# Kernel tuning notes

Hardware: AMD Instinct MI355X
Metric: run time of the kernel (lower is better)

Reference implementation:

```python
import jax, jax.numpy as jnp
import numpy as np

EPS = 1e-6
GROUPS = 8


def setup_inputs() -> dict:
    key = jax.random.key(0)
    ks = jax.random.split(key, 8)
    B, C, H, W = 4, 128, 64, 64
    s = 1.0 / np.sqrt(C)
    return {
        "x": jax.random.normal(ks[0], (B, C, H, W), jnp.float32),
        "gn_scale": jnp.ones((C,), jnp.float32),
        "gn_bias": jnp.zeros((C,), jnp.float32),
        "wq": jax.random.normal(ks[1], (C, C), jnp.float32) * s,
        "bq": jnp.zeros((C,), jnp.float32),
        "wk": jax.random.normal(ks[2], (C, C), jnp.float32) * s,
        "bk": jnp.zeros((C,), jnp.float32),
        "wv": jax.random.normal(ks[3], (C, C), jnp.float32) * s,
        "bv": jnp.zeros((C,), jnp.float32),
        "wp": jax.random.normal(ks[4], (C, C), jnp.float32) * s,
        "bp": jnp.zeros((C,), jnp.float32),
    }


def _group_norm(x, scale, bias):
    B, C, H, W = x.shape
    g = x.reshape(B, GROUPS, C // GROUPS, H * W)
    mu = g.mean(axis=(2, 3), keepdims=True)
    var = g.var(axis=(2, 3), keepdims=True)
    g = (g - mu) * jax.lax.rsqrt(var + EPS)
    g = g.reshape(B, C, H, W)
    return g * scale[None, :, None, None] + bias[None, :, None, None]


def reference(x, gn_scale, gn_bias, wq, bq, wk, bk, wv, bv, wp, bp):
    B, C, H, W = x.shape
    N = H * W
    h = _group_norm(x, gn_scale, gn_bias).reshape(B, C, N)
    # 1x1 convs == channel matmuls: (C_out, C_in) x (B, C_in, N)
    q = jnp.einsum('oc,bcn->bon', wq, h) + bq[None, :, None]
    k = jnp.einsum('oc,bcn->bon', wk, h) + bk[None, :, None]
    v = jnp.einsum('oc,bcn->bon', wv, h) + bv[None, :, None]
    # scores: (B, N, N), w[b,n,m] = sum_c q[b,c,n] k[b,c,m]
    w = jnp.einsum('bcn,bcm->bnm', q, k) * (C ** -0.5)
    w = jax.nn.softmax(w, axis=-1)
    # h_[b,c,n] = sum_m w[b,n,m] v[b,c,m]
    h_ = jnp.einsum('bnm,bcm->bcn', w, v)
    out = jnp.einsum('oc,bcn->bon', wp, h_) + bp[None, :, None]
    return x + out.reshape(B, C, H, W)
```

## Files before the change

kernel.cpp:

```cpp
#include <hip/hip_runtime.h>
#include <math.h>

#define B_ 4
#define C_ 128
#define N_ 4096
#define NSPLIT 4
#define MT 32
#define PLD 40
#define HLD 136
#define VTLD 24

typedef float floatx4 __attribute__((ext_vector_type(4)));
typedef short bf16x8 __attribute__((ext_vector_type(8)));

__device__ __forceinline__ ushort f2bf(float f) {
  unsigned u = __float_as_uint(f);
  return (ushort)((u + 0x7FFF + ((u >> 16) & 1)) >> 16);
}
__device__ __forceinline__ float bf2f(ushort u) {
  return __uint_as_float(((unsigned)u) << 16);
}
__device__ __forceinline__ unsigned pkbf(float a, float b) {
  return __builtin_amdgcn_perm(__float_as_uint(a) + 0x8000u,
                               __float_as_uint(b) + 0x8000u, 0x07060302u);
}
__device__ __forceinline__ float fexp2(float x) {
#if __has_builtin(__builtin_amdgcn_exp2f)
  return __builtin_amdgcn_exp2f(x);
#else
  return exp2f(x);
#endif
}
__device__ __forceinline__ void gl2lds16(const ushort* g, ushort* l) {
  __builtin_amdgcn_global_load_lds(
      (const __attribute__((address_space(1))) void*)g,
      (__attribute__((address_space(3))) void*)l, 16, 0, 0);
}

__global__ __launch_bounds__(256) void prep_kernel(
    const float* __restrict__ x, float* __restrict__ gstat,
    const float* __restrict__ wq, const float* __restrict__ wk,
    const float* __restrict__ wv, const float* __restrict__ wp,
    ushort* __restrict__ wB) {
  if (blockIdx.x >= 256) {
    int i = (blockIdx.x - 256) * 256 + threadIdx.x;
    int m = i >> 14, j = i & 16383;
    const float* src = (m == 0) ? wq : (m == 1) ? wk : (m == 2) ? wv : wp;
    wB[i] = f2bf(src[j]);
    return;
  }
  int b = blockIdx.x >> 6, g = (blockIdx.x >> 3) & 7, part = blockIdx.x & 7;
  const float4* xp = (const float4*)(x + (size_t)(b * C_ + g * 16) * N_) + part * 2048;
  float s = 0.f, ss = 0.f;
  for (int i = threadIdx.x; i < 2048; i += 256) {
    float4 v = xp[i];
    s += v.x + v.y + v.z + v.w;
    ss += v.x * v.x + v.y * v.y + v.z * v.z + v.w * v.w;
  }
  #pragma unroll
  for (int o = 32; o > 0; o >>= 1) {
    s += __shfl_down(s, o, 64);
    ss += __shfl_down(ss, o, 64);
  }
  __shared__ float rs[4], rss[4];
  int wid = threadIdx.x >> 6, lane = threadIdx.x & 63;
  if (lane == 0) { rs[wid] = s; rss[wid] = ss; }
  __syncthreads();
  if (threadIdx.x == 0) {
    int slot = (b * 8 + g) * 8 + part;
    gstat[slot]       = rs[0] + rs[1] + rs[2] + rs[3];
    gstat[256 + slot] = rss[0] + rss[1] + rss[2] + rss[3];
  }
}

__global__ __launch_bounds__(256) void gnqkv_kernel(
    const float* __restrict__ x, const float* __restrict__ gstat,
    const float* __restrict__ scale, const float* __restrict__ bias,
    const ushort* __restrict__ wB,
    const float* __restrict__ bq, const float* __restrict__ bk,
    const float* __restrict__ bv,
    ushort* __restrict__ qT, ushort* __restrict__ kT, ushort* __restrict__ vB) {
  __shared__ __align__(16) ushort hs[16][HLD];
  __shared__ __align__(16) ushort Qt[16][HLD];
  __shared__ __align__(16) ushort Kt[16][HLD];
  __shared__ __align__(16) ushort Vt[128][VTLD];
  __shared__ float sSc[C_], sBi[C_];
  int tid = threadIdx.x;
  int b = blockIdx.x >> 8;
  int n0 = (blockIdx.x & 255) * 16;
  if (tid < 128) {
    int g = tid >> 4;
    float S = 0.f, SS = 0.f;
    #pragma unroll
    for (int p = 0; p < 8; ++p) {
      S  += gstat[(b * 8 + g) * 8 + p];
      SS += gstat[256 + (b * 8 + g) * 8 + p];
    }
    float mu = S * (1.f / 65536.f);
    float var = SS * (1.f / 65536.f) - mu * mu;
    float rstd = rsqrtf(var + 1e-6f);
    float sc = scale[tid] * rstd;
    sSc[tid] = sc;
    sBi[tid] = bias[tid] - mu * sc;
  }
  __syncthreads();
  #pragma unroll
  for (int k2 = 0; k2 < 2; ++k2) {
    int i = tid + k2 * 256;
    int c = i >> 2, n4 = i & 3;
    float4 v = *(const float4*)(x + (size_t)(b * C_ + c) * N_ + n0 + n4 * 4);
    float sc = sSc[c], bi = sBi[c];
    hs[n4 * 4 + 0][c] = f2bf(v.x * sc + bi);
    hs[n4 * 4 + 1][c] = f2bf(v.y * sc + bi);
    hs[n4 * 4 + 2][c] = f2bf(v.z * sc + bi);
    hs[n4 * 4 + 3][c] = f2bf(v.w * sc + bi);
  }
  __syncthreads();
  int lane = tid & 63, w = tid >> 6;
  int col = lane & 15, quad = lane >> 4;
  int oh = w * 32;
  bf16x8 hf[4];
  #pragma unroll
  for (int kc = 0; kc < 4; ++kc)
    hf[kc] = *(const bf16x8*)&hs[col][kc * 32 + quad * 8];
  const ushort* Wq = wB;
  const ushort* Wk = wB + 16384;
  const ushort* Wv = wB + 32768;
  const float scl = 0.12751879752224991f;
  #pragma unroll
  for (int ot = 0; ot < 2; ++ot) {
    int o0 = oh + ot * 16;
    floatx4 aq = (floatx4)0.f, ak = (floatx4)0.f, av = (floatx4)0.f;
    #pragma unroll
    for (int kc = 0; kc < 4; ++kc) {
      int wo = (o0 + col) * C_ + kc * 32 + quad * 8;
      aq = __builtin_amdgcn_mfma_f32_16x16x32_bf16(*(const bf16x8*)&Wq[wo], hf[kc], aq, 0, 0, 0);
      ak = __builtin_amdgcn_mfma_f32_16x16x32_bf16(*(const bf16x8*)&Wk[wo], hf[kc], ak, 0, 0, 0);
      av = __builtin_amdgcn_mfma_f32_16x16x32_bf16(*(const bf16x8*)&Wv[wo], hf[kc], av, 0, 0, 0);
    }
    float4 bqv = *(const float4*)&bq[o0 + quad * 4];
    float4 bkv = *(const float4*)&bk[o0 + quad * 4];
    float4 bvv = *(const float4*)&bv[o0 + quad * 4];
    uint2 qs = { pkbf((aq[1] + bqv.y) * scl, (aq[0] + bqv.x) * scl),
                 pkbf((aq[3] + bqv.w) * scl, (aq[2] + bqv.z) * scl) };
    uint2 ks = { pkbf(ak[1] + bkv.y, ak[0] + bkv.x),
                 pkbf(ak[3] + bkv.w, ak[2] + bkv.z) };
    *(uint2*)&Qt[col][o0 + quad * 4] = qs;
    *(uint2*)&Kt[col][o0 + quad * 4] = ks;
    float vv[4] = {av[0] + bvv.x, av[1] + bvv.y, av[2] + bvv.z, av[3] + bvv.w};
    #pragma unroll
    for (int r = 0; r < 4; ++r)
      Vt[o0 + quad * 4 + r][col] = f2bf(vv[r]);
  }
  __syncthreads();
  {
    int row = tid >> 4, seg = tid & 15;
    size_t dst = ((size_t)b * N_ + n0 + row) * C_ + seg * 8;
    *(uint4*)(qT + dst) = *(const uint4*)&Qt[row][seg * 8];
    *(uint4*)(kT + dst) = *(const uint4*)&Kt[row][seg * 8];
  }
  {
    int o = tid >> 1, seg = tid & 1;
    *(uint4*)(vB + ((size_t)b * C_ + o) * N_ + n0 + seg * 8) = *(const uint4*)&Vt[o][seg * 8];
  }
}

__global__ __launch_bounds__(512, 4) void attn_kernel(
    const ushort* __restrict__ qT, const ushort* __restrict__ kT,
    const ushort* __restrict__ vB, ushort* __restrict__ Op,
    float* __restrict__ Lv) {
  __shared__ __align__(16) ushort Ks[2][MT * 128];
  __shared__ __align__(16) ushort Vs[2][C_ * MT];
  __shared__ __align__(16) ushort Ps[2][128 * PLD];
  __shared__ float lpart[8][2][16];
  int sp = blockIdx.x & 3;
  int qblk = (blockIdx.x >> 2) & 31;
  int b = blockIdx.x >> 7;
  int n0 = qblk * 128;
  int tid = threadIdx.x, lane = tid & 63, w = tid >> 6;
  int col = lane & 15, quad = lane >> 4;
  int wu = __builtin_amdgcn_readfirstlane(w);
  int mtw = w & 1, qg = w >> 1;
  int qh = w & 1, cq = w >> 1;
  const ushort* kTb = kT + (size_t)b * N_ * C_;
  const ushort* vBb = vB + (size_t)b * C_ * N_;

  bf16x8 qf[2][4];
  #pragma unroll
  for (int qt = 0; qt < 2; ++qt)
    #pragma unroll
    for (int kc = 0; kc < 4; ++kc)
      qf[qt][kc] = *(const bf16x8*)(qT + ((size_t)b * N_ + n0 + qg * 32 + qt * 16 + col) * C_ + kc * 32 + quad * 8);

  floatx4 Oacc[4][2];
  #pragma unroll
  for (int qt = 0; qt < 4; ++qt)
    #pragma unroll
    for (int ct = 0; ct < 2; ++ct) Oacc[qt][ct] = (floatx4)0.f;
  float lacc[2] = {0.f, 0.f};

  const int m00 = sp * 1024;

  const ushort* kgp;
  const ushort* vgp;
  {
    int r = wu * 4 + (lane >> 4);
    int pos = (lane & 15) ^ (r & 7);
    kgp = kTb + (size_t)(m00 + r) * 128 + pos * 8;
    int c = wu * 16 + (lane >> 2);
    int mc = (lane & 3) ^ ((lane >> 3) & 3);
    vgp = vBb + (size_t)c * N_ + m00 + mc * 8;
  }

  #define STAGE(buf)                                   \
    {                                                  \
      gl2lds16(kgp, &Ks[buf][wu * 512]);               \
      gl2lds16(vgp, &Vs[buf][wu * 512]);               \
      kgp += MT * 128;                                 \
      vgp += MT;                                       \
    }

  #define S_COMPUTE(KsB, st)                                                          \
    {                                                                                 \
      int row = mtw * 16 + col;                                                       \
      bf16x8 kf[4];                                                                   \
      _Pragma("unroll")                                                               \
      for (int kc = 0; kc < 4; ++kc)                                                  \
        kf[kc] = *(const bf16x8*)&(KsB)[row * 128 + (((4 * kc + quad) ^ (col & 7)) * 8)]; \
      __builtin_amdgcn_s_setprio(1);                                                  \
      _Pragma("unroll")                                                               \
      for (int qt = 0; qt < 2; ++qt) {                                                \
        floatx4 acc = (floatx4)0.f;                                                   \
        _Pragma("unroll")                                                             \
        for (int kc = 0; kc < 4; ++kc)                                                \
          acc = __builtin_amdgcn_mfma_f32_16x16x32_bf16(kf[kc], qf[qt][kc], acc, 0, 0, 0); \
        st[qt] = acc;                                                                 \
      }                                                                               \
      __builtin_amdgcn_s_setprio(0);                                                  \
    }

  #define SOFTMAX_WRITE(PsB, st)                                                      \
    {                                                                                 \
      _Pragma("unroll")                                                               \
      for (int qt = 0; qt < 2; ++qt) {                                                \
        int prow = (qg * 32 + qt * 16 + col) * PLD + mtw * 16;                        \
        float p0 = fexp2(st[qt][0]);                                                  \
        float p1 = fexp2(st[qt][1]);                                                  \
        float p2 = fexp2(st[qt][2]);                                                  \
        float p3 = fexp2(st[qt][3]);                                                  \
        uint2 pk = { pkbf(p1, p0), pkbf(p3, p2) };                                    \
        *(uint2*)&(PsB)[prow + quad * 4] = pk;                                        \
        lacc[qt] += (p0 + p1) + (p2 + p3);                                            \
      }                                                                               \
    }

  #define V_LOAD(VsB, vfp)                                                            \
    {                                                                                 \
      _Pragma("unroll")                                                               \
      for (int ct = 0; ct < 2; ++ct)                                                  \
        vfp[ct] = *(const bf16x8*)&(VsB)[(cq * 32 + ct * 16 + col) * MT +             \
                                         ((quad ^ ((col >> 1) & 3)) * 8)];            \
    }

  #define PV_COMPUTE(PsB, vfp)                                                        \
    {                                                                                 \
      __builtin_amdgcn_s_setprio(1);                                                  \
      _Pragma("unroll")                                                               \
      for (int qt = 0; qt < 4; ++qt) {                                                \
        bf16x8 pf = *(const bf16x8*)&(PsB)[(qh * 64 + qt * 16 + col) * PLD + quad * 8]; \
        _Pragma("unroll")                                                             \
        for (int ct = 0; ct < 2; ++ct)                                                \
          Oacc[qt][ct] = __builtin_amdgcn_mfma_f32_16x16x32_bf16(pf, vfp[ct], Oacc[qt][ct], 0, 0, 0); \
      }                                                                               \
      __builtin_amdgcn_s_setprio(0);                                                  \
    }

  floatx4 st[2];
  bf16x8 vfp[2];

  STAGE(0);
  __syncthreads();

  STAGE(1);
  S_COMPUTE(Ks[0], st);
  SOFTMAX_WRITE(Ps[0], st);
  V_LOAD(Vs[0], vfp);
  __syncthreads();

  for (int t = 1; t < 31; ++t) {
    STAGE((t + 1) & 1);
    S_COMPUTE(Ks[t & 1], st);
    PV_COMPUTE(Ps[(t - 1) & 1], vfp);
    SOFTMAX_WRITE(Ps[t & 1], st);
    V_LOAD(Vs[t & 1], vfp);
    __syncthreads();
  }

  S_COMPUTE(Ks[1], st);
  PV_COMPUTE(Ps[0], vfp);
  SOFTMAX_WRITE(Ps[1], st);
  V_LOAD(Vs[1], vfp);
  __syncthreads();

  PV_COMPUTE(Ps[1], vfp);

  ushort* OpB = Op + (((size_t)sp * B_ + b) * N_ + n0) * C_;
  #pragma unroll
  for (int qt = 0; qt < 4; ++qt)
    #pragma unroll
    for (int ct = 0; ct < 2; ++ct)
      #pragma unroll
      for (int r = 0; r < 4; ++r)
        OpB[(size_t)(qh * 64 + qt * 16 + quad * 4 + r) * C_ + cq * 32 + ct * 16 + col] =
            f2bf(Oacc[qt][ct][r]);
  #pragma unroll
  for (int qt = 0; qt < 2; ++qt) {
    float lsum = lacc[qt];
    lsum += __shfl_xor(lsum, 16, 64);
    lsum += __shfl_xor(lsum, 32, 64);
    if (quad == 0) lpart[w][qt][col] = lsum;
  }
  __syncthreads();
  if ((w & 1) == 0 && quad == 0) {
    #pragma unroll
    for (int qt = 0; qt < 2; ++qt) {
      int idx = b * N_ + n0 + (w >> 1) * 32 + qt * 16 + col;
      Lv[(size_t)sp * (B_ * N_) + idx] = lpart[w][qt][col] + lpart[w + 1][qt][col];
    }
  }
}

__global__ __launch_bounds__(256) void mergeproj_kernel(
    const ushort* __restrict__ Op, const float* __restrict__ Lv,
    const ushort* __restrict__ wpB, const float* __restrict__ bp,
    const float* __restrict__ x, float* __restrict__ out) {
  __shared__ __align__(16) ushort tile[16 * HLD];
  int tid = threadIdx.x;
  int b = blockIdx.x >> 8;
  int n0 = (blockIdx.x & 255) * 16;
  {
    int n = tid >> 4, cc = tid & 15;
    int nIdx = b * N_ + n0 + n;
    float den = Lv[0 * (B_ * N_) + nIdx] + Lv[1 * (B_ * N_) + nIdx] +
                Lv[2 * (B_ * N_) + nIdx] + Lv[3 * (B_ * N_) + nIdx];
    float inv = 1.f / den;
    float o[8];
    #pragma unroll
    for (int j = 0; j < 8; ++j) o[j] = 0.f;
    #pragma unroll
    for (int sp = 0; sp < NSPLIT; ++sp) {
      uint4 d = *(const uint4*)&Op[((size_t)sp * (B_ * N_) + nIdx) * C_ + cc * 8];
      unsigned dd[4] = {d.x, d.y, d.z, d.w};
      #pragma unroll
      for (int j = 0; j < 4; ++j) {
        o[j * 2]     += bf2f((ushort)(dd[j] & 0xFFFF));
        o[j * 2 + 1] += bf2f((ushort)(dd[j] >> 16));
      }
    }
    uint4 res;
    res.x = pkbf(o[1] * inv, o[0] * inv);
    res.y = pkbf(o[3] * inv, o[2] * inv);
    res.z = pkbf(o[5] * inv, o[4] * inv);
    res.w = pkbf(o[7] * inv, o[6] * inv);
    *(uint4*)&tile[n * HLD + cc * 8] = res;
  }
  __syncthreads();
  int lane = tid & 63, w = tid >> 6;
  int col = lane & 15, quad = lane >> 4;
  int oh = w * 32;
  bf16x8 hf[4];
  #pragma unroll
  for (int kc = 0; kc < 4; ++kc)
    hf[kc] = *(const bf16x8*)&tile[col * HLD + kc * 32 + quad * 8];
  #pragma unroll
  for (int ot = 0; ot < 2; ++ot) {
    int o0 = oh + ot * 16;
    floatx4 acc = (floatx4)0.f;
    #pragma unroll
    for (int kc = 0; kc < 4; ++kc) {
      int wo = (o0 + col) * C_ + kc * 32 + quad * 8;
      acc = __builtin_amdgcn_mfma_f32_16x16x32_bf16(*(const bf16x8*)&wpB[wo], hf[kc], acc, 0, 0, 0);
    }
    float4 bpv = *(const float4*)&bp[o0 + quad * 4];
    float bb[4] = {bpv.x, bpv.y, bpv.z, bpv.w};
    #pragma unroll
    for (int r = 0; r < 4; ++r) {
      size_t idx = ((size_t)b * C_ + o0 + quad * 4 + r) * N_ + n0 + col;
      out[idx] = acc[r] + bb[r] + x[idx];
    }
  }
}

extern "C" void kernel_launch(void* const* d_in, const int* in_sizes, int n_in,
                              void* d_out, int out_size, void* d_ws, size_t ws_size,
                              hipStream_t stream) {
  const float* x        = (const float*)d_in[0];
  const float* gn_scale = (const float*)d_in[1];
  const float* gn_bias  = (const float*)d_in[2];
  const float* wq = (const float*)d_in[3];
  const float* bq = (const float*)d_in[4];
  const float* wk = (const float*)d_in[5];
  const float* bk = (const float*)d_in[6];
  const float* wv = (const float*)d_in[7];
  const float* bv = (const float*)d_in[8];
  const float* wp = (const float*)d_in[9];
  const float* bp = (const float*)d_in[10];
  float* out = (float*)d_out;

  char* ws = (char*)d_ws;
  float*  Lv    = (float*)(ws + 262144);
  ushort* wB    = (ushort*)(ws + 524288);
  float*  gstat = (float*)(ws + 655360);
  ushort* qT    = (ushort*)(ws + (4u << 20));
  ushort* kT    = (ushort*)(ws + (8u << 20));
  ushort* vB    = (ushort*)(ws + (12u << 20));
  ushort* Op    = (ushort*)(ws + (16u << 20));
  ushort* wpB   = wB + 49152;

  prep_kernel<<<512, 256, 0, stream>>>(x, gstat, wq, wk, wv, wp, wB);
  gnqkv_kernel<<<1024, 256, 0, stream>>>(x, gstat, gn_scale, gn_bias, wB, bq, bk, bv, qT, kT, vB);
  attn_kernel<<<512, 512, 0, stream>>>(qT, kT, vB, Op, Lv);
  mergeproj_kernel<<<1024, 256, 0, stream>>>(Op, Lv, wpB, bp, x, out);
}
```

Before: 148.8 us.

## Halve attention query tile to 64 rows and double grid blocks

Each attention block now handles 64 query rows instead of 128, so the grid doubles to 1024 blocks. Each wave computes one 16-row score tile and a 32x32 output slice, which cuts registers and LDS per block and spreads work over more blocks for better occupancy and CU balance. In exchange, every K/V tile is staged from global memory into LDS twice as often per query, doubling K/V traffic and lowering MFMA work per staged tile.

```diff
diff --git a/kernel.cpp b/kernel.cpp
--- a/kernel.cpp
+++ b/kernel.cpp
@@ -171,33 +171,31 @@
     float* __restrict__ Lv) {
   __shared__ __align__(16) ushort Ks[2][MT * 128];
   __shared__ __align__(16) ushort Vs[2][C_ * MT];
-  __shared__ __align__(16) ushort Ps[2][128 * PLD];
-  __shared__ float lpart[8][2][16];
+  __shared__ __align__(16) ushort Ps[2][64 * PLD];
+  __shared__ float lpart[8][16];
   int sp = blockIdx.x & 3;
-  int qblk = (blockIdx.x >> 2) & 31;
-  int b = blockIdx.x >> 7;
-  int n0 = qblk * 128;
+  int qblk = (blockIdx.x >> 2) & 63;
+  int b = blockIdx.x >> 8;
+  int n0 = qblk * 64;
   int tid = threadIdx.x, lane = tid & 63, w = tid >> 6;
   int col = lane & 15, quad = lane >> 4;
   int wu = __builtin_amdgcn_readfirstlane(w);
-  int mtw = w & 1, qg = w >> 1;
-  int qh = w & 1, cq = w >> 1;
+  int mt = w & 1, qs = w >> 1;
+  int qp = w & 1, cq = w >> 1;
   const ushort* kTb = kT + (size_t)b * N_ * C_;
   const ushort* vBb = vB + (size_t)b * C_ * N_;
 
-  bf16x8 qf[2][4];
-  #pragma unroll
-  for (int qt = 0; qt < 2; ++qt)
-    #pragma unroll
-    for (int kc = 0; kc < 4; ++kc)
-      qf[qt][kc] = *(const bf16x8*)(qT + ((size_t)b * N_ + n0 + qg * 32 + qt * 16 + col) * C_ + kc * 32 + quad * 8);
-
-  floatx4 Oacc[4][2];
-  #pragma unroll
-  for (int qt = 0; qt < 4; ++qt)
-    #pragma unroll
-    for (int ct = 0; ct < 2; ++ct) Oacc[qt][ct] = (floatx4)0.f;
-  float lacc[2] = {0.f, 0.f};
+  bf16x8 qf[4];
+  #pragma unroll
+  for (int kc = 0; kc < 4; ++kc)
+    qf[kc] = *(const bf16x8*)(qT + ((size_t)b * N_ + n0 + qs * 16 + col) * C_ + kc * 32 + quad * 8);
+
+  floatx4 Oacc[2][2];
+  #pragma unroll
+  for (int qt2 = 0; qt2 < 2; ++qt2)
+    #pragma unroll
+    for (int ct = 0; ct < 2; ++ct) Oacc[qt2][ct] = (floatx4)0.f;
+  float lacc = 0.f;
 
   const int m00 = sp * 1024;
 
@@ -222,36 +220,30 @@
 
   #define S_COMPUTE(KsB, st)                                                          \
     {                                                                                 \
-      int row = mtw * 16 + col;                                                       \
+      int row = mt * 16 + col;                                                        \
       bf16x8 kf[4];                                                                   \
       _Pragma("unroll")                                                               \
       for (int kc = 0; kc < 4; ++kc)                                                  \
         kf[kc] = *(const bf16x8*)&(KsB)[row * 128 + (((4 * kc + quad) ^ (col & 7)) * 8)]; \
       __builtin_amdgcn_s_setprio(1);                                                  \
+      floatx4 acc = (floatx4)0.f;                                                     \
       _Pragma("unroll")                                                               \
-      for (int qt = 0; qt < 2; ++qt) {                                                \
-        floatx4 acc = (floatx4)0.f;                                                   \
-        _Pragma("unroll")                                                             \
-        for (int kc = 0; kc < 4; ++kc)                                                \
-          acc = __builtin_amdgcn_mfma_f32_16x16x32_bf16(kf[kc], qf[qt][kc], acc, 0, 0, 0); \
-        st[qt] = acc;                                                                 \
-      }                                                                               \
+      for (int kc = 0; kc < 4; ++kc)                                                  \
+        acc = __builtin_amdgcn_mfma_f32_16x16x32_bf16(kf[kc], qf[kc], acc, 0, 0, 0);  \
       __builtin_amdgcn_s_setprio(0);                                                  \
+      st = acc;                                                                       \
     }
 
   #define SOFTMAX_WRITE(PsB, st)                                                      \
     {                                                                                 \
-      _Pragma("unroll")                                                               \
-      for (int qt = 0; qt < 2; ++qt) {                                                \
-        int prow = (qg * 32 + qt * 16 + col) * PLD + mtw * 16;                        \
-        float p0 = fexp2(st[qt][0]);                                                  \
-        float p1 = fexp2(st[qt][1]);                                                  \
-        float p2 = fexp2(st[qt][2]);                                                  \
-        float p3 = fexp2(st[qt][3]);                                                  \
-        uint2 pk = { pkbf(p1, p0), pkbf(p3, p2) };                                    \
-        *(uint2*)&(PsB)[prow + quad * 4] = pk;                                        \
-        lacc[qt] += (p0 + p1) + (p2 + p3);                                            \
-      }                                                                               \
+      int prow = (qs * 16 + col) * PLD + mt * 16;                                     \
+      float p0 = fexp2(st[0]);                                                        \
+      float p1 = fexp2(st[1]);                                                        \
+      float p2 = fexp2(st[2]);                                                        \
+      float p3 = fexp2(st[3]);                                                        \
+      uint2 pk = { pkbf(p1, p0), pkbf(p3, p2) };                                      \
+      *(uint2*)&(PsB)[prow + quad * 4] = pk;                                          \
+      lacc += (p0 + p1) + (p2 + p3);                                                  \
     }
 
   #define V_LOAD(VsB, vfp)                                                            \
@@ -266,16 +258,16 @@
     {                                                                                 \
       __builtin_amdgcn_s_setprio(1);                                                  \
       _Pragma("unroll")                                                               \
-      for (int qt = 0; qt < 4; ++qt) {                                                \
-        bf16x8 pf = *(const bf16x8*)&(PsB)[(qh * 64 + qt * 16 + col) * PLD + quad * 8]; \
+      for (int qt2 = 0; qt2 < 2; ++qt2) {                                             \
+        bf16x8 pf = *(const bf16x8*)&(PsB)[(qp * 32 + qt2 * 16 + col) * PLD + quad * 8]; \
         _Pragma("unroll")                                                             \
         for (int ct = 0; ct < 2; ++ct)                                                \
-          Oacc[qt][ct] = __builtin_amdgcn_mfma_f32_16x16x32_bf16(pf, vfp[ct], Oacc[qt][ct], 0, 0, 0); \
+          Oacc[qt2][ct] = __builtin_amdgcn_mfma_f32_16x16x32_bf16(pf, vfp[ct], Oacc[qt2][ct], 0, 0, 0); \
       }                                                                               \
       __builtin_amdgcn_s_setprio(0);                                                  \
     }
 
-  floatx4 st[2];
+  floatx4 st;
   bf16x8 vfp[2];
 
   STAGE(0);
@@ -306,27 +298,23 @@
 
   ushort* OpB = Op + (((size_t)sp * B_ + b) * N_ + n0) * C_;
   #pragma unroll
-  for (int qt = 0; qt < 4; ++qt)
+  for (int qt2 = 0; qt2 < 2; ++qt2)
     #pragma unroll
     for (int ct = 0; ct < 2; ++ct)
       #pragma unroll
       for (int r = 0; r < 4; ++r)
-        OpB[(size_t)(qh * 64 + qt * 16 + quad * 4 + r) * C_ + cq * 32 + ct * 16 + col] =
-            f2bf(Oacc[qt][ct][r]);
-  #pragma unroll
-  for (int qt = 0; qt < 2; ++qt) {
-    float lsum = lacc[qt];
+        OpB[(size_t)(qp * 32 + qt2 * 16 + quad * 4 + r) * C_ + cq * 32 + ct * 16 + col] =
+            f2bf(Oacc[qt2][ct][r]);
+  {
+    float lsum = lacc;
     lsum += __shfl_xor(lsum, 16, 64);
     lsum += __shfl_xor(lsum, 32, 64);
-    if (quad == 0) lpart[w][qt][col] = lsum;
+    if (quad == 0) lpart[w][col] = lsum;
   }
   __syncthreads();
   if ((w & 1) == 0 && quad == 0) {
-    #pragma unroll
-    for (int qt = 0; qt < 2; ++qt) {
-      int idx = b * N_ + n0 + (w >> 1) * 32 + qt * 16 + col;
-      Lv[(size_t)sp * (B_ * N_) + idx] = lpart[w][qt][col] + lpart[w + 1][qt][col];
-    }
+    int idx = b * N_ + n0 + (w >> 1) * 16 + col;
+    Lv[(size_t)sp * (B_ * N_) + idx] = lpart[w][col] + lpart[w + 1][col];
   }
 }
 
@@ -419,6 +407,6 @@
 
   prep_kernel<<<512, 256, 0, stream>>>(x, gstat, wq, wk, wv, wp, wB);
   gnqkv_kernel<<<1024, 256, 0, stream>>>(x, gstat, gn_scale, gn_bias, wB, bq, bk, bv, qT, kT, vB);
-  attn_kernel<<<512, 512, 0, stream>>>(qT, kT, vB, Op, Lv);
+  attn_kernel<<<1024, 512, 0, stream>>>(qT, kT, vB, Op, Lv);
   mergeproj_kernel<<<1024, 256, 0, stream>>>(Op, Lv, wpB, bp, x, out);
 }
```

After: 158.0 us. 1.06x slower.
